# Kernel tuning notes

Hardware: AMD Instinct MI355X
Metric: run time of the kernel (lower is better)

Reference implementation:

```python
import jax, jax.numpy as jnp
import numpy as np

EPS = 1e-5
NV, NF, NV_PREV = 40962, 81920, 10242  # icosphere level 6 / level 5
B, HALF, OUT = 2, 64, 64


def setup_inputs() -> dict:
    key = jax.random.key(0)
    ks = jax.random.split(key, 32)
    rn = lambda i, shape, s=1.0: jax.random.normal(ks[i], shape, dtype=jnp.float32) * s
    ri = lambda i, shape, hi: jax.random.randint(ks[i], shape, 0, hi, dtype=jnp.int32)
    ru = lambda i, shape: jax.random.uniform(ks[i], shape, dtype=jnp.float32, minval=0.5, maxval=1.5)
    s_up = 1.0 / np.sqrt(HALF * 4)   # torch uniform(-stdv, stdv) scale analog
    s_c1 = 1.0 / np.sqrt(2 * HALF)
    s_c3 = 1.0 / np.sqrt(OUT)
    return {
        'x1': rn(0, (B, HALF, NV_PREV)),
        'x2': rn(1, (B, HALF, NV)),
        'G_cols': ri(2, (3 * NF, 3), NV), 'G_vals': rn(3, (3 * NF, 3), 0.1),
        'L_cols': ri(4, (NV, 7), NV), 'L_vals': rn(5, (NV, 7), 0.1),
        'F2V_cols': ri(6, (NV, 6), NF), 'F2V_vals': rn(7, (NV, 6), 0.3),
        'EW': rn(8, (NF, 3)), 'NS': rn(9, (NF, 3)),
        'v2p': jnp.arange(NV_PREV, dtype=jnp.int32),
        'up_coeffs': rn(10, (HALF, HALF, 4), s_up), 'up_bias': rn(11, (HALF,), s_up),
        'c2_coeffs': rn(12, (OUT, OUT, 4), 1.0 / np.sqrt(OUT * 4)), 'c2_bias': rn(13, (OUT,), 1.0 / np.sqrt(OUT * 4)),
        'conv1_w': rn(14, (OUT, 2 * HALF), s_c1), 'conv1_b': rn(15, (OUT,), s_c1),
        'conv3_w': rn(16, (OUT, OUT), s_c3), 'conv3_b': rn(17, (OUT,), s_c3),
        'convs_w': rn(18, (OUT, 2 * HALF), s_c1), 'convs_b': rn(19, (OUT,), s_c1),
        'bn1_g': ru(20, (OUT,)), 'bn1_b': rn(21, (OUT,), 0.1),
        'bn2_g': ru(22, (OUT,)), 'bn2_b': rn(23, (OUT,), 0.1),
        'bn3_g': ru(24, (OUT,)), 'bn3_b': rn(25, (OUT,), 0.1),
        'bns_g': ru(26, (OUT,)), 'bns_b': rn(27, (OUT,), 0.1),
    }


def spmm_ell(x, cols, vals):
    """x: (B,C,V), cols/vals: (R,K) fixed-nnz-per-row sparse matrix -> (B,C,R)."""
    return jnp.einsum('bcrk,rk->bcr', x[:, :, cols], vals)


def mesh_conv(x, coeffs, bias, G_cols, G_vals, L_cols, L_vals, F2V_cols, F2V_vals, EW, NS):
    b, c, v = x.shape
    # gradient on faces: (B,C,3*NF) -> (B,C,NF,3)
    gf = spmm_ell(x, G_cols, G_vals).reshape(b, c, 3, -1).transpose(0, 1, 3, 2)
    lap = spmm_ell(x, L_cols, L_vals)                                 # (B,C,V)
    gv_ew = spmm_ell(jnp.sum(gf * EW, axis=-1), F2V_cols, F2V_vals)   # (B,C,V)
    gv_ns = spmm_ell(jnp.sum(gf * NS, axis=-1), F2V_cols, F2V_vals)   # (B,C,V)
    feat = jnp.stack([x, lap, gv_ew, gv_ns], axis=-1)                 # (B,C,V,4)
    return jnp.einsum('bivk,oik->bov', feat, coeffs) + bias[:, None]


def bn(x, g, b):
    # training-mode BatchNorm1d over (batch, vertex) dims, biased variance
    m = jnp.mean(x, axis=(0, 2), keepdims=True)
    v = jnp.mean((x - m) ** 2, axis=(0, 2), keepdims=True)
    return g[:, None] * (x - m) / jnp.sqrt(v + EPS) + b[:, None]


def pconv(x, w, b):
    # 1x1 Conv1d
    return jnp.einsum('bcv,oc->bov', x, w) + b[:, None]


def reference(x1, x2, G_cols, G_vals, L_cols, L_vals, F2V_cols, F2V_vals, EW, NS, v2p,
              up_coeffs, up_bias, c2_coeffs, c2_bias, conv1_w, conv1_b, conv3_w, conv3_b,
              convs_w, convs_b, bn1_g, bn1_b, bn2_g, bn2_b, bn3_g, bn3_b, bns_g, bns_b):
    sp = (G_cols, G_vals, L_cols, L_vals, F2V_cols, F2V_vals, EW, NS)
    # MeshConv_transpose: pad with ONES (as in torch source) then mesh conv
    b, c, _ = x1.shape
    xin = jnp.ones((b, c, NV), dtype=x1.dtype).at[:, :, v2p].set(x1)
    xu = mesh_conv(xin, up_coeffs, up_bias, *sp)
    x = jnp.concatenate([x2, xu], axis=1)  # (B, in_ch, NV)
    # ResPoolBlock (coarsen=False, diff_chan=True)
    h = jax.nn.relu(bn(pconv(x, conv1_w, conv1_b), bn1_g, bn1_b))
    h = jax.nn.relu(bn(mesh_conv(h, c2_coeffs, c2_bias, *sp), bn2_g, bn2_b))
    h = bn(pconv(h, conv3_w, conv3_b), bn3_g, bn3_b)
    s = bn(pconv(x, convs_w, convs_b), bns_g, bns_b)
    return jax.nn.relu(h + s)
```

## Files before the change

kernel.cpp:

```cpp
#include <hip/hip_runtime.h>

typedef unsigned short u16;
typedef unsigned int u32;

constexpr int kNV  = 40962;
constexpr int kNF  = 81920;
constexpr int kNVP = 10242;
constexpr int kB   = 2;
constexpr float kEPS  = 1e-5f;
constexpr int kBNN   = kB * kNV;
constexpr float kInvN = 1.0f / (float)kBNN;
constexpr int kTiles = (kBNN + 15) / 16;

typedef __attribute__((ext_vector_type(8))) short bf16x8;
typedef __attribute__((ext_vector_type(4))) float f32x4;
union U4 { uint4 u; bf16x8 h; };

__device__ __forceinline__ float bflo(u32 u) { return __uint_as_float(u << 16); }
__device__ __forceinline__ float bfhi(u32 u) { return __uint_as_float(u & 0xffff0000u); }
__device__ __forceinline__ u32 packbf(float a, float b) {
    u32 ua = __float_as_uint(a), ub = __float_as_uint(b);
    ua += 0x7fffu + ((ua >> 16) & 1u);
    ub += 0x7fffu + ((ub >> 16) & 1u);
    return (ua >> 16) | (ub & 0xffff0000u);
}
__device__ __forceinline__ u16 bf16r(float a) {
    u32 ua = __float_as_uint(a);
    ua += 0x7fffu + ((ua >> 16) & 1u);
    return (u16)(ua >> 16);
}
__device__ __forceinline__ float b2f(u16 u) { return __uint_as_float(((u32)u) << 16); }

__global__ void zero_stats_k(float* stats) {
    int t = threadIdx.x;
    if (t < 512) stats[t] = 0.f;
}

__global__ __launch_bounds__(256) void build_facetab_k(
    const int* __restrict__ Gc, const float* __restrict__ Gv,
    const float* __restrict__ ew, const float* __restrict__ ns,
    uint4* __restrict__ tab)
{
    int idx = blockIdx.x * 256 + threadIdx.x;
    if (idx >= kNF * 9) return;
    int f = idx / 9, jk = idx - f * 9;
    int j = jk / 3, k = jk - j * 3;
    int r = j * kNF + f;
    float gv = Gv[r * 3 + k];
    tab[idx] = make_uint4((u32)Gc[r * 3 + k],
                          __float_as_uint(gv * ew[f * 3 + j]),
                          __float_as_uint(gv * ns[f * 3 + j]), 0u);
}

__global__ __launch_bounds__(256) void pack_coeffs_k(const float* __restrict__ coeffs,
                                                     u16* __restrict__ Bg)
{
    int idx = blockIdx.x * 256 + threadIdx.x;
    if (idx >= 256 * 64) return;
    int k = idx >> 6, col = idx & 63;
    int s = k >> 5, kg = (k >> 3) & 3, jj = k & 7;
    Bg[((s * 4 + kg) * 64 + col) * 8 + jj] =
        bf16r(coeffs[((size_t)col * 64 + (k >> 2)) * 4 + (k & 3)]);
}

__global__ __launch_bounds__(256) void transpose_in_k(const float* __restrict__ x1,
                                                      const float* __restrict__ x2,
                                                      u16* __restrict__ xin16,
                                                      u16* __restrict__ Xc) {
    __shared__ float t1[64 * 65];
    __shared__ float t2[64 * 65];
    const int tilesPerB = (kNV + 63) / 64;
    int tile = blockIdx.x % tilesPerB;
    int b    = blockIdx.x / tilesPerB;
    int v0   = tile * 64;
    int tid  = threadIdx.x;
    bool hasX1 = v0 < kNVP;
#pragma unroll
    for (int r = 0; r < 16; ++r) {
        int idx = r * 256 + tid;
        int c = idx >> 6, vl = idx & 63;
        int v = v0 + vl;
        if (v < kNV) {
            t2[vl * 65 + c] = x2[(size_t)(b * 64 + c) * kNV + v];
            if (hasX1) t1[vl * 65 + c] = (v < kNVP) ? x1[(size_t)(b * 64 + c) * kNVP + v] : 1.0f;
        }
    }
    __syncthreads();
#pragma unroll
    for (int r = 0; r < 16; ++r) {
        int idx = r * 256 + tid;
        int vl = idx >> 6, c = idx & 63;
        int v = v0 + vl;
        if (v < kNV) {
            Xc[(size_t)(b * kNV + v) * 128 + c]   = bf16r(t2[vl * 65 + c]);
            xin16[(size_t)(b * kNV + v) * 64 + c] = hasX1 ? bf16r(t1[vl * 65 + c]) : (u16)0x3f80;
        }
    }
}

template <bool BN>
__global__ __launch_bounds__(256) void face_k(
    const u16* __restrict__ src,
    const uint4* __restrict__ tab,
    const float* __restrict__ st, const float* __restrict__ bg, const float* __restrict__ bb,
    u32* __restrict__ gegn)
{
    int lane = threadIdx.x & 63;
    int cl = lane & 31, half = lane >> 5;
    int c0 = 2 * cl;
    int wave = blockIdx.x * 4 + (threadIdx.x >> 6);
    int nW   = gridDim.x * 4;
    float sc0 = 0.f, sh0 = 0.f, sc1 = 0.f, sh1 = 0.f;
    if constexpr (BN) {
        float m0 = st[c0] * kInvN, m1 = st[c0 + 1] * kInvN;
        float v0 = st[64 + c0] * kInvN - m0 * m0;
        float v1 = st[64 + c0 + 1] * kInvN - m1 * m1;
        sc0 = bg[c0] * rsqrtf(v0 + kEPS);     sh0 = bb[c0] - m0 * sc0;
        sc1 = bg[c0 + 1] * rsqrtf(v1 + kEPS); sh1 = bb[c0 + 1] - m1 * sc1;
    }
    const int nG = (kB * kNF) / 8;
    for (int g = wave; g < nG; g += nW) {
        int t0 = g * 8;
#pragma unroll
        for (int p = 0; p < 4; ++p) {
            int task = t0 + 2 * p + half;
            int b = task >= kNF;
            int f = task - (b ? kNF : 0);
            const u16* sb = src + (size_t)b * kNV * 64;
            const uint4* tf = tab + (size_t)f * 9;
            float aE0 = 0.f, aE1 = 0.f, aN0 = 0.f, aN1 = 0.f;
#pragma unroll
            for (int jk = 0; jk < 9; ++jk) {
                uint4 tb = tf[jk];
                float wE = __uint_as_float(tb.y), wN = __uint_as_float(tb.z);
                u32 xv = *(const u32*)&sb[(size_t)tb.x * 64 + c0];
                float x0 = bflo(xv), x1 = bfhi(xv);
                if constexpr (BN) {
                    x0 = fmaf(x0, sc0, sh0); x0 = x0 > 0.f ? x0 : 0.f;
                    x1 = fmaf(x1, sc1, sh1); x1 = x1 > 0.f ? x1 : 0.f;
                }
                aE0 = fmaf(wE, x0, aE0); aE1 = fmaf(wE, x1, aE1);
                aN0 = fmaf(wN, x0, aN0); aN1 = fmaf(wN, x1, aN1);
            }
            *(uint2*)&gegn[(size_t)task * 64 + c0] =
                make_uint2(packbf(aE0, aN0), packbf(aE1, aN1));
        }
    }
}

template <bool STATS, bool BN, bool OUT16>
__global__ __launch_bounds__(256, 2) void vertex_fused_k(
    const u16* __restrict__ src,
    const u32* __restrict__ gegn,
    const int* __restrict__ Lc, const float* __restrict__ Lv,
    const int* __restrict__ Fc, const float* __restrict__ Fv,
    const uint4* __restrict__ Bg,
    const float* __restrict__ bias,
    const float* __restrict__ st, const float* __restrict__ bg, const float* __restrict__ bbn,
    void* __restrict__ out_, int outStride, float* __restrict__ stats)
{
    __shared__ __align__(16) uint2 feat[4][16][64];
    __shared__ float sred[STATS ? 4 * 128 : 4];
    int tid   = threadIdx.x;
    int lane  = tid & 63;
    int cl = lane & 31, half = lane >> 5;
    int c0 = 2 * cl;
    int wslot = tid >> 6;
    float sc0 = 0.f, sh0 = 0.f, sc1 = 0.f, sh1 = 0.f;
    if constexpr (BN) {
        float m0 = st[c0] * kInvN, m1 = st[c0 + 1] * kInvN;
        float v0 = st[64 + c0] * kInvN - m0 * m0;
        float v1 = st[64 + c0 + 1] * kInvN - m1 * m1;
        sc0 = bg[c0] * rsqrtf(v0 + kEPS);     sh0 = bbn[c0] - m0 * sc0;
        sc1 = bg[c0 + 1] * rsqrtf(v1 + kEPS); sh1 = bbn[c0 + 1] - m1 * sc1;
    }
    int tA = lane & 15, kg = lane >> 4;
    const int amask = (tA & 3) << 3;
    float bias_w[4];
#pragma unroll
    for (int nf = 0; nf < 4; ++nf) bias_w[nf] = bias[nf * 16 + tA];
    float s_[4] = {0.f, 0.f, 0.f, 0.f}, sq_[4] = {0.f, 0.f, 0.f, 0.f};

    int wave = blockIdx.x * 4 + wslot;
    int nW   = gridDim.x * 4;

    for (int tile = wave; tile < kTiles; tile += nW) {
        int base = tile * 16;
#pragma unroll 4
        for (int p = 0; p < 8; ++p) {
            int t = 2 * p + half;
            int task = base + t;
            float x0 = 0.f, x1 = 0.f, l0 = 0.f, l1 = 0.f;
            float e0 = 0.f, e1 = 0.f, n0 = 0.f, n1 = 0.f;
            if (task < kBNN) {
                int b = task >= kNV;
                int v = task - (b ? kNV : 0);
                const u16* sb = src + (size_t)b * kNV * 64;
                const u32* gb = gegn + (size_t)b * kNF * 64;
                u32 xv = *(const u32*)&src[(size_t)task * 64 + c0];
                x0 = bflo(xv); x1 = bfhi(xv);
                if constexpr (BN) {
                    x0 = fmaf(x0, sc0, sh0); x0 = x0 > 0.f ? x0 : 0.f;
                    x1 = fmaf(x1, sc1, sh1); x1 = x1 > 0.f ? x1 : 0.f;
                }
#pragma unroll
                for (int k = 0; k < 7; ++k) {
                    int col = Lc[v * 7 + k];
                    float w = Lv[v * 7 + k];
                    u32 lv = *(const u32*)&sb[(size_t)col * 64 + c0];
                    float y0 = bflo(lv), y1 = bfhi(lv);
                    if constexpr (BN) {
                        y0 = fmaf(y0, sc0, sh0); y0 = y0 > 0.f ? y0 : 0.f;
                        y1 = fmaf(y1, sc1, sh1); y1 = y1 > 0.f ? y1 : 0.f;
                    }
                    l0 = fmaf(w, y0, l0); l1 = fmaf(w, y1, l1);
                }
#pragma unroll
                for (int k = 0; k < 6; ++k) {
                    int col = Fc[v * 6 + k];
                    float w = Fv[v * 6 + k];
                    uint2 gv = *(const uint2*)&gb[(size_t)col * 64 + c0];
                    e0 = fmaf(w, bflo(gv.x), e0); n0 = fmaf(w, bfhi(gv.x), n0);
                    e1 = fmaf(w, bflo(gv.y), e1); n1 = fmaf(w, bfhi(gv.y), n1);
                }
            }
            int cs = c0 ^ ((t & 3) << 3);
            *(uint4*)&feat[wslot][t][cs] =
                make_uint4(packbf(x0, l0), packbf(e0, n0), packbf(x1, l1), packbf(e1, n1));
        }
        f32x4 z = {0.f, 0.f, 0.f, 0.f};
        f32x4 acc[4]; acc[0] = z; acc[1] = z; acc[2] = z; acc[3] = z;
#pragma unroll
        for (int sl = 0; sl < 8; ++sl) {
            int i0 = sl * 8 + kg * 2;
            U4 a; a.u = *(const uint4*)&feat[wslot][tA][i0 ^ amask];
#pragma unroll
            for (int nf = 0; nf < 4; ++nf) {
                U4 bb; bb.u = Bg[(sl * 4 + kg) * 64 + nf * 16 + tA];
                acc[nf] = __builtin_amdgcn_mfma_f32_16x16x32_bf16(a.h, bb.h, acc[nf], 0, 0, 0);
            }
        }
#pragma unroll
        for (int nf = 0; nf < 4; ++nf) {
#pragma unroll
            for (int r = 0; r < 4; ++r) {
                int task = base + kg * 4 + r;
                if (task < kBNN) {
                    float val = acc[nf][r] + bias_w[nf];
                    int col = nf * 16 + tA;
                    if constexpr (OUT16)
                        ((u16*)out_)[(size_t)task * outStride + col] = bf16r(val);
                    else
                        ((float*)out_)[(size_t)task * outStride + col] = val;
                    if constexpr (STATS) { s_[nf] += val; sq_[nf] += val * val; }
                }
            }
        }
    }
    if constexpr (STATS) {
#pragma unroll
        for (int nf = 0; nf < 4; ++nf) {
            s_[nf]  += __shfl_xor(s_[nf], 16, 64);  s_[nf]  += __shfl_xor(s_[nf], 32, 64);
            sq_[nf] += __shfl_xor(sq_[nf], 16, 64); sq_[nf] += __shfl_xor(sq_[nf], 32, 64);
        }
        if (lane < 16) {
#pragma unroll
            for (int nf = 0; nf < 4; ++nf) {
                sred[wslot * 128 + nf * 16 + lane]      = s_[nf];
                sred[wslot * 128 + 64 + nf * 16 + lane] = sq_[nf];
            }
        }
        __syncthreads();
        if (wslot == 0) {
            float S = 0.f, SQ = 0.f;
#pragma unroll
            for (int w = 0; w < 4; ++w) {
                S  += sred[w * 128 + lane];
                SQ += sred[w * 128 + 64 + lane];
            }
            atomicAdd(&stats[lane], S);
            atomicAdd(&stats[64 + lane], SQ);
        }
    }
}

__global__ __launch_bounds__(512) void pconv_dual_k(
    const u16* __restrict__ Xc,
    const float* __restrict__ W1, const float* __restrict__ b1,
    const float* __restrict__ W2, const float* __restrict__ b2,
    u16* __restrict__ O1, u16* __restrict__ O2,
    float* __restrict__ stats1, float* __restrict__ stats2)
{
    __shared__ __align__(16) u16 Bl[128 * 128];
    __shared__ float sred[8 * 256];
    int tid = threadIdx.x;
    for (int idx = tid; idx < 128 * 128; idx += 512) {
        int k = idx >> 7, col = idx & 127;
        int s = k >> 5, kg = (k >> 3) & 3, jj = k & 7;
        float v = (col < 64) ? W1[(size_t)col * 128 + k] : W2[(size_t)(col - 64) * 128 + k];
        Bl[((s * 4 + kg) * 128 + (col ^ kg)) * 8 + jj] = bf16r(v);
    }
    __syncthreads();

    int lane = tid & 63, wslot = tid >> 6;
    int tA = lane & 15, kg = lane >> 4;
    float bias_w[8];
#pragma unroll
    for (int nf = 0; nf < 8; ++nf)
        bias_w[nf] = (nf < 4) ? b1[nf * 16 + tA] : b2[(nf - 4) * 16 + tA];
    float s_[8] = {0.f}, sq_[8] = {0.f};

    int wave = blockIdx.x * 8 + wslot;
    int nW   = gridDim.x * 8;
    for (int tile = wave; tile < kTiles; tile += nW) {
        int base = tile * 16;
        int taskA = min(base + tA, kBNN - 1);
        f32x4 zz = {0.f, 0.f, 0.f, 0.f};
        f32x4 acc[8];
#pragma unroll
        for (int nf = 0; nf < 8; ++nf) acc[nf] = zz;
#pragma unroll
        for (int s = 0; s < 4; ++s) {
            U4 a; a.u = *(const uint4*)&Xc[(size_t)taskA * 128 + s * 32 + kg * 8];
#pragma unroll
            for (int nf = 0; nf < 8; ++nf) {
                int colb = nf * 16 + tA;
                U4 bb; bb.u = *(const uint4*)&Bl[((s * 4 + kg) * 128 + (colb ^ kg)) * 8];
                acc[nf] = __builtin_amdgcn_mfma_f32_16x16x32_bf16(a.h, bb.h, acc[nf], 0, 0, 0);
            }
        }
#pragma unroll
        for (int nf = 0; nf < 8; ++nf) {
#pragma unroll
            for (int r = 0; r < 4; ++r) {
                int task = base + kg * 4 + r;
                if (task < kBNN) {
                    float val = acc[nf][r] + bias_w[nf];
                    if (nf < 4) O1[(size_t)task * 64 + nf * 16 + tA] = bf16r(val);
                    else        O2[(size_t)task * 64 + (nf - 4) * 16 + tA] = bf16r(val);
                    s_[nf] += val; sq_[nf] += val * val;
                }
            }
        }
    }
#pragma unroll
    for (int nf = 0; nf < 8; ++nf) {
        s_[nf]  += __shfl_xor(s_[nf], 16, 64);  s_[nf]  += __shfl_xor(s_[nf], 32, 64);
        sq_[nf] += __shfl_xor(sq_[nf], 16, 64); sq_[nf] += __shfl_xor(sq_[nf], 32, 64);
    }
    if (lane < 16) {
#pragma unroll
        for (int nf = 0; nf < 8; ++nf) {
            sred[wslot * 256 + nf * 16 + lane]       = s_[nf];
            sred[wslot * 256 + 128 + nf * 16 + lane] = sq_[nf];
        }
    }
    __syncthreads();
    if (wslot == 0) {
        float S = 0.f, SQ = 0.f;
#pragma unroll
        for (int w = 0; w < 8; ++w) {
            S  += sred[w * 256 + lane];
            SQ += sred[w * 256 + 128 + lane];
        }
        atomicAdd(&stats1[lane], S);
        atomicAdd(&stats1[64 + lane], SQ);
    } else if (wslot == 1) {
        float S = 0.f, SQ = 0.f;
#pragma unroll
        for (int w = 0; w < 8; ++w) {
            S  += sred[w * 256 + 64 + lane];
            SQ += sred[w * 256 + 128 + 64 + lane];
        }
        atomicAdd(&stats2[lane], S);
        atomicAdd(&stats2[64 + lane], SQ);
    }
}

__global__ __launch_bounds__(512) void pconv3_k(
    const u16* __restrict__ P2,
    const float* __restrict__ st2, const float* __restrict__ g2, const float* __restrict__ b2n,
    const float* __restrict__ W, const float* __restrict__ bW,
    u16* __restrict__ O, float* __restrict__ stats)
{
    __shared__ __align__(16) u16 Bl[64 * 64];
    __shared__ float sred[8 * 128];
    int tid = threadIdx.x;
    for (int idx = tid; idx < 64 * 64; idx += 512) {
        int k = idx >> 6, col = idx & 63;
        int s = k >> 5, kg = (k >> 3) & 3, jj = k & 7;
        Bl[((s * 4 + kg) * 64 + (col ^ kg)) * 8 + jj] = bf16r(W[(size_t)col * 64 + k]);
    }
    __syncthreads();

    int lane = tid & 63, wslot = tid >> 6;
    int tA = lane & 15, kg = lane >> 4;
    float scA[2][8], shA[2][8];
#pragma unroll
    for (int s = 0; s < 2; ++s)
#pragma unroll
        for (int j = 0; j < 8; ++j) {
            int ch = s * 32 + kg * 8 + j;
            float m   = st2[ch] * kInvN;
            float var = st2[64 + ch] * kInvN - m * m;
            float sc  = g2[ch] * rsqrtf(var + kEPS);
            scA[s][j] = sc;
            shA[s][j] = b2n[ch] - m * sc;
        }
    float bias_w[4];
#pragma unroll
    for (int nf = 0; nf < 4; ++nf) bias_w[nf] = bW[nf * 16 + tA];
    float s_[4] = {0.f}, sq_[4] = {0.f};

    int wave = blockIdx.x * 8 + wslot;
    int nW   = gridDim.x * 8;
    for (int tile = wave; tile < kTiles; tile += nW) {
        int base = tile * 16;
        int taskA = min(base + tA, kBNN - 1);
        f32x4 zz = {0.f, 0.f, 0.f, 0.f};
        f32x4 acc[4]; acc[0] = zz; acc[1] = zz; acc[2] = zz; acc[3] = zz;
#pragma unroll
        for (int s = 0; s < 2; ++s) {
            U4 raw; raw.u = *(const uint4*)&P2[(size_t)taskA * 64 + s * 32 + kg * 8];
            u32 w_[4];
#pragma unroll
            for (int p = 0; p < 4; ++p) {
                u32 word = (p < 2) ? ((p == 0) ? raw.u.x : raw.u.y) : ((p == 2) ? raw.u.z : raw.u.w);
                float t0 = fmaf(bflo(word), scA[s][2 * p],     shA[s][2 * p]);     t0 = t0 > 0.f ? t0 : 0.f;
                float t1 = fmaf(bfhi(word), scA[s][2 * p + 1], shA[s][2 * p + 1]); t1 = t1 > 0.f ? t1 : 0.f;
                w_[p] = packbf(t0, t1);
            }
            U4 a; a.u = make_uint4(w_[0], w_[1], w_[2], w_[3]);
#pragma unroll
            for (int nf = 0; nf < 4; ++nf) {
                int colb = nf * 16 + tA;
                U4 bb; bb.u = *(const uint4*)&Bl[((s * 4 + kg) * 64 + (colb ^ kg)) * 8];
                acc[nf] = __builtin_amdgcn_mfma_f32_16x16x32_bf16(a.h, bb.h, acc[nf], 0, 0, 0);
            }
        }
#pragma unroll
        for (int nf = 0; nf < 4; ++nf) {
#pragma unroll
            for (int r = 0; r < 4; ++r) {
                int task = base + kg * 4 + r;
                if (task < kBNN) {
                    float val = acc[nf][r] + bias_w[nf];
                    O[(size_t)task * 64 + nf * 16 + tA] = bf16r(val);
                    s_[nf] += val; sq_[nf] += val * val;
                }
            }
        }
    }
#pragma unroll
    for (int nf = 0; nf < 4; ++nf) {
        s_[nf]  += __shfl_xor(s_[nf], 16, 64);  s_[nf]  += __shfl_xor(s_[nf], 32, 64);
        sq_[nf] += __shfl_xor(sq_[nf], 16, 64); sq_[nf] += __shfl_xor(sq_[nf], 32, 64);
    }
    if (lane < 16) {
#pragma unroll
        for (int nf = 0; nf < 4; ++nf) {
            sred[wslot * 128 + nf * 16 + lane]      = s_[nf];
            sred[wslot * 128 + 64 + nf * 16 + lane] = sq_[nf];
        }
    }
    __syncthreads();
    if (wslot == 0) {
        float S = 0.f, SQ = 0.f;
#pragma unroll
        for (int w = 0; w < 8; ++w) {
            S  += sred[w * 128 + lane];
            SQ += sred[w * 128 + 64 + lane];
        }
        atomicAdd(&stats[lane], S);
        atomicAdd(&stats[64 + lane], SQ);
    }
}

__global__ __launch_bounds__(256) void final_k(
    const u16* __restrict__ P3, const u16* __restrict__ S,
    const float* __restrict__ st3, const float* __restrict__ stS,
    const float* __restrict__ g3, const float* __restrict__ b3,
    const float* __restrict__ gs, const float* __restrict__ bs,
    float* __restrict__ out)
{
    __shared__ float lds[64 * 65];
    const int tilesPerB = (kNV + 63) / 64;
    int tile = blockIdx.x % tilesPerB;
    int b    = blockIdx.x / tilesPerB;
    int v0   = tile * 64;
    int tid  = threadIdx.x;
#pragma unroll
    for (int r = 0; r < 16; ++r) {
        int idx = r * 256 + tid;
        int vl = idx >> 6, o = idx & 63;
        int v = v0 + vl;
        if (v < kNV) {
            float m3  = st3[o] * kInvN;
            float vr3 = st3[64 + o] * kInvN - m3 * m3;
            float sc3 = g3[o] * rsqrtf(vr3 + kEPS);
            float sh3 = b3[o] - m3 * sc3;
            float mS  = stS[o] * kInvN;
            float vrS = stS[64 + o] * kInvN - mS * mS;
            float scS = gs[o] * rsqrtf(vrS + kEPS);
            float shS = bs[o] - mS * scS;
            size_t base = (size_t)(b * kNV + v) * 64 + o;
            float val = fmaf(b2f(P3[base]), sc3, sh3) + fmaf(b2f(S[base]), scS, shS);
            lds[vl * 65 + o] = val > 0.f ? val : 0.f;
        }
    }
    __syncthreads();
#pragma unroll
    for (int r = 0; r < 16; ++r) {
        int idx = r * 256 + tid;
        int o = idx >> 6, vl = idx & 63;
        int v = v0 + vl;
        if (v < kNV) out[(size_t)(b * 64 + o) * kNV + v] = lds[vl * 65 + o];
    }
}

extern "C" void kernel_launch(void* const* d_in, const int* in_sizes, int n_in,
                              void* d_out, int out_size, void* d_ws, size_t ws_size,
                              hipStream_t stream) {
    const float* x1  = (const float*)d_in[0];
    const float* x2  = (const float*)d_in[1];
    const int*   Gc  = (const int*)d_in[2];
    const float* Gv  = (const float*)d_in[3];
    const int*   Lc  = (const int*)d_in[4];
    const float* Lv  = (const float*)d_in[5];
    const int*   Fc  = (const int*)d_in[6];
    const float* Fv  = (const float*)d_in[7];
    const float* ew  = (const float*)d_in[8];
    const float* ns  = (const float*)d_in[9];
    const float* upC = (const float*)d_in[11];
    const float* upB = (const float*)d_in[12];
    const float* c2C = (const float*)d_in[13];
    const float* c2B = (const float*)d_in[14];
    const float* w1  = (const float*)d_in[15];
    const float* b1  = (const float*)d_in[16];
    const float* w3  = (const float*)d_in[17];
    const float* b3  = (const float*)d_in[18];
    const float* wsw = (const float*)d_in[19];
    const float* wsb = (const float*)d_in[20];
    const float* bn1g = (const float*)d_in[21];
    const float* bn1b = (const float*)d_in[22];
    const float* bn2g = (const float*)d_in[23];
    const float* bn2b = (const float*)d_in[24];
    const float* bn3g = (const float*)d_in[25];
    const float* bn3b = (const float*)d_in[26];
    const float* bnsg = (const float*)d_in[27];
    const float* bnsb = (const float*)d_in[28];

    float* ws = (float*)d_ws;
    float* stats = ws;
    size_t off = 512;
    u16* Xc    = (u16*)(ws + off); off += (size_t)kBNN * 64;
    u16* xin16 = (u16*)(ws + off); off += (size_t)kBNN * 32;
    u32* gegn  = (u32*)(ws + off); off += (size_t)kB * kNF * 64;
    u16* P1    = (u16*)(ws + off); off += (size_t)kBNN * 32;
    u16* Sbuf  = (u16*)(ws + off); off += (size_t)kBNN * 32;
    u16* P2    = (u16*)(ws + off); off += (size_t)kBNN * 32;
    u16* P3    = (u16*)(ws + off); off += (size_t)kBNN * 32;
    uint4* faceTab = (uint4*)(ws + off); off += (size_t)kNF * 9 * 4;
    u16* BgUp = (u16*)(ws + off); off += 256 * 64 / 2;
    u16* BgC2 = (u16*)(ws + off); off += 256 * 64 / 2;
    float* out = (float*)d_out;

    zero_stats_k<<<1, 512, 0, stream>>>(stats);
    build_facetab_k<<<(kNF * 9 + 255) / 256, 256, 0, stream>>>(Gc, Gv, ew, ns, faceTab);
    pack_coeffs_k<<<64, 256, 0, stream>>>(upC, BgUp);
    pack_coeffs_k<<<64, 256, 0, stream>>>(c2C, BgC2);
    transpose_in_k<<<2 * 641, 256, 0, stream>>>(x1, x2, xin16, Xc);
    face_k<false><<<2048, 256, 0, stream>>>(xin16, faceTab,
                                            nullptr, nullptr, nullptr, gegn);
    vertex_fused_k<false, false, true><<<1280, 256, 0, stream>>>(
        xin16, gegn, Lc, Lv, Fc, Fv, (const uint4*)BgUp, upB,
        nullptr, nullptr, nullptr, (void*)(Xc + 64), 128, nullptr);
    pconv_dual_k<<<512, 512, 0, stream>>>(Xc, w1, b1, wsw, wsb, P1, Sbuf,
                                          stats + 0 * 128, stats + 3 * 128);
    face_k<true><<<2048, 256, 0, stream>>>(P1, faceTab,
                                           stats + 0 * 128, bn1g, bn1b, gegn);
    vertex_fused_k<true, true, true><<<1280, 256, 0, stream>>>(
        P1, gegn, Lc, Lv, Fc, Fv, (const uint4*)BgC2, c2B,
        stats + 0 * 128, bn1g, bn1b, P2, 64, stats + 1 * 128);
    pconv3_k<<<512, 512, 0, stream>>>(P2, stats + 1 * 128, bn2g, bn2b,
                                      w3, b3, P3, stats + 2 * 128);
    final_k<<<2 * 641, 256, 0, stream>>>(P3, Sbuf, stats + 2 * 128, stats + 3 * 128,
                                         bn3g, bn3b, bnsg, bnsb, out);
}
```

Measured before the change: 261.2 us.

## Widen per-lane gathers to four channels and pack vertex sparse tables

```diff
diff --git a/kernel.cpp b/kernel.cpp
--- a/kernel.cpp
+++ b/kernel.cpp
@@ -50,6 +50,28 @@
     tab[idx] = make_uint4((u32)Gc[r * 3 + k],
                           __float_as_uint(gv * ew[f * 3 + j]),
                           __float_as_uint(gv * ns[f * 3 + j]), 0u);
+}
+
+__global__ __launch_bounds__(256) void build_vtab_k(
+    const int* __restrict__ Lc, const float* __restrict__ Lv,
+    const int* __restrict__ Fc, const float* __restrict__ Fv,
+    u32* __restrict__ vtab)
+{
+    int v = blockIdx.x * 256 + threadIdx.x;
+    if (v >= kNV) return;
+    u32* d = vtab + (size_t)v * 32;
+#pragma unroll
+    for (int k = 0; k < 7; ++k) {
+        d[k]      = (u32)Lc[v * 7 + k];
+        d[16 + k] = __float_as_uint(Lv[v * 7 + k]);
+    }
+#pragma unroll
+    for (int k = 0; k < 6; ++k) {
+        d[7 + k]  = (u32)Fc[v * 6 + k];
+        d[23 + k] = __float_as_uint(Fv[v * 6 + k]);
+    }
+    d[13] = 0; d[14] = 0; d[15] = 0;
+    d[29] = 0; d[30] = 0; d[31] = 0;
 }
 
 __global__ __launch_bounds__(256) void pack_coeffs_k(const float* __restrict__ coeffs,
@@ -106,44 +128,48 @@
     u32* __restrict__ gegn)
 {
     int lane = threadIdx.x & 63;
-    int cl = lane & 31, half = lane >> 5;
-    int c0 = 2 * cl;
+    int q  = lane >> 4;
+    int c0 = 4 * (lane & 15);
     int wave = blockIdx.x * 4 + (threadIdx.x >> 6);
     int nW   = gridDim.x * 4;
-    float sc0 = 0.f, sh0 = 0.f, sc1 = 0.f, sh1 = 0.f;
+    float sc[4], sh[4];
     if constexpr (BN) {
-        float m0 = st[c0] * kInvN, m1 = st[c0 + 1] * kInvN;
-        float v0 = st[64 + c0] * kInvN - m0 * m0;
-        float v1 = st[64 + c0 + 1] * kInvN - m1 * m1;
-        sc0 = bg[c0] * rsqrtf(v0 + kEPS);     sh0 = bb[c0] - m0 * sc0;
-        sc1 = bg[c0 + 1] * rsqrtf(v1 + kEPS); sh1 = bb[c0 + 1] - m1 * sc1;
-    }
-    const int nG = (kB * kNF) / 8;
+#pragma unroll
+        for (int j = 0; j < 4; ++j) {
+            float m   = st[c0 + j] * kInvN;
+            float var = st[64 + c0 + j] * kInvN - m * m;
+            sc[j] = bg[c0 + j] * rsqrtf(var + kEPS);
+            sh[j] = bb[c0 + j] - m * sc[j];
+        }
+    }
+    const int nG = (kB * kNF) / 16;
     for (int g = wave; g < nG; g += nW) {
-        int t0 = g * 8;
+        int t0 = g * 16;
 #pragma unroll
         for (int p = 0; p < 4; ++p) {
-            int task = t0 + 2 * p + half;
+            int task = t0 + 4 * p + q;
             int b = task >= kNF;
             int f = task - (b ? kNF : 0);
             const u16* sb = src + (size_t)b * kNV * 64;
             const uint4* tf = tab + (size_t)f * 9;
-            float aE0 = 0.f, aE1 = 0.f, aN0 = 0.f, aN1 = 0.f;
+            float aE[4] = {0.f, 0.f, 0.f, 0.f}, aN[4] = {0.f, 0.f, 0.f, 0.f};
 #pragma unroll
             for (int jk = 0; jk < 9; ++jk) {
                 uint4 tb = tf[jk];
                 float wE = __uint_as_float(tb.y), wN = __uint_as_float(tb.z);
-                u32 xv = *(const u32*)&sb[(size_t)tb.x * 64 + c0];
-                float x0 = bflo(xv), x1 = bfhi(xv);
-                if constexpr (BN) {
-                    x0 = fmaf(x0, sc0, sh0); x0 = x0 > 0.f ? x0 : 0.f;
-                    x1 = fmaf(x1, sc1, sh1); x1 = x1 > 0.f ? x1 : 0.f;
+                uint2 xv = *(const uint2*)&sb[(size_t)tb.x * 64 + c0];
+                float x_[4] = {bflo(xv.x), bfhi(xv.x), bflo(xv.y), bfhi(xv.y)};
+#pragma unroll
+                for (int j = 0; j < 4; ++j) {
+                    float x = x_[j];
+                    if constexpr (BN) { x = fmaf(x, sc[j], sh[j]); x = x > 0.f ? x : 0.f; }
+                    aE[j] = fmaf(wE, x, aE[j]);
+                    aN[j] = fmaf(wN, x, aN[j]);
                 }
-                aE0 = fmaf(wE, x0, aE0); aE1 = fmaf(wE, x1, aE1);
-                aN0 = fmaf(wN, x0, aN0); aN1 = fmaf(wN, x1, aN1);
-            }
-            *(uint2*)&gegn[(size_t)task * 64 + c0] =
-                make_uint2(packbf(aE0, aN0), packbf(aE1, aN1));
+            }
+            *(uint4*)&gegn[(size_t)task * 64 + c0] =
+                make_uint4(packbf(aE[0], aN[0]), packbf(aE[1], aN[1]),
+                           packbf(aE[2], aN[2]), packbf(aE[3], aN[3]));
         }
     }
 }
@@ -152,8 +178,7 @@
 __global__ __launch_bounds__(256, 2) void vertex_fused_k(
     const u16* __restrict__ src,
     const u32* __restrict__ gegn,
-    const int* __restrict__ Lc, const float* __restrict__ Lv,
-    const int* __restrict__ Fc, const float* __restrict__ Fv,
+    const u32* __restrict__ vtab,
     const uint4* __restrict__ Bg,
     const float* __restrict__ bias,
     const float* __restrict__ st, const float* __restrict__ bg, const float* __restrict__ bbn,
@@ -163,16 +188,18 @@
     __shared__ float sred[STATS ? 4 * 128 : 4];
     int tid   = threadIdx.x;
     int lane  = tid & 63;
-    int cl = lane & 31, half = lane >> 5;
-    int c0 = 2 * cl;
+    int q  = lane >> 4;
+    int c0 = 4 * (lane & 15);
     int wslot = tid >> 6;
-    float sc0 = 0.f, sh0 = 0.f, sc1 = 0.f, sh1 = 0.f;
+    float sc[4], sh[4];
     if constexpr (BN) {
-        float m0 = st[c0] * kInvN, m1 = st[c0 + 1] * kInvN;
-        float v0 = st[64 + c0] * kInvN - m0 * m0;
-        float v1 = st[64 + c0 + 1] * kInvN - m1 * m1;
-        sc0 = bg[c0] * rsqrtf(v0 + kEPS);     sh0 = bbn[c0] - m0 * sc0;
-        sc1 = bg[c0 + 1] * rsqrtf(v1 + kEPS); sh1 = bbn[c0 + 1] - m1 * sc1;
+#pragma unroll
+        for (int j = 0; j < 4; ++j) {
+            float m   = st[c0 + j] * kInvN;
+            float var = st[64 + c0 + j] * kInvN - m * m;
+            sc[j] = bg[c0 + j] * rsqrtf(var + kEPS);
+            sh[j] = bbn[c0 + j] - m * sc[j];
+        }
     }
     int tA = lane & 15, kg = lane >> 4;
     const int amask = (tA & 3) << 3;
@@ -186,47 +213,68 @@
 
     for (int tile = wave; tile < kTiles; tile += nW) {
         int base = tile * 16;
-#pragma unroll 4
-        for (int p = 0; p < 8; ++p) {
-            int t = 2 * p + half;
+#pragma unroll
+        for (int p = 0; p < 4; ++p) {
+            int t = 4 * p + q;
             int task = base + t;
-            float x0 = 0.f, x1 = 0.f, l0 = 0.f, l1 = 0.f;
-            float e0 = 0.f, e1 = 0.f, n0 = 0.f, n1 = 0.f;
+            float x_[4] = {0.f, 0.f, 0.f, 0.f}, l_[4] = {0.f, 0.f, 0.f, 0.f};
+            float e_[4] = {0.f, 0.f, 0.f, 0.f}, n_[4] = {0.f, 0.f, 0.f, 0.f};
             if (task < kBNN) {
                 int b = task >= kNV;
                 int v = task - (b ? kNV : 0);
                 const u16* sb = src + (size_t)b * kNV * 64;
                 const u32* gb = gegn + (size_t)b * kNF * 64;
-                u32 xv = *(const u32*)&src[(size_t)task * 64 + c0];
-                x0 = bflo(xv); x1 = bfhi(xv);
-                if constexpr (BN) {
-                    x0 = fmaf(x0, sc0, sh0); x0 = x0 > 0.f ? x0 : 0.f;
-                    x1 = fmaf(x1, sc1, sh1); x1 = x1 > 0.f ? x1 : 0.f;
+                const u32* vt = vtab + (size_t)v * 32;
+                uint4  I0 = *(const uint4*)&vt[0];
+                uint4  I1 = *(const uint4*)&vt[4];
+                uint4  I2 = *(const uint4*)&vt[8];
+                u32    I3 = vt[12];
+                float4 W0 = *(const float4*)&vt[16];
+                float4 W1 = *(const float4*)&vt[20];
+                float4 W2 = *(const float4*)&vt[24];
+                float  W3 = __uint_as_float(vt[28]);
+                u32 Lcols[7] = {I0.x, I0.y, I0.z, I0.w, I1.x, I1.y, I1.z};
+                float Lw[7]  = {W0.x, W0.y, W0.z, W0.w, W1.x, W1.y, W1.z};
+                u32 Fcols[6] = {I1.w, I2.x, I2.y, I2.z, I2.w, I3};
+                float Fw[6]  = {W1.w, W2.x, W2.y, W2.z, W2.w, W3};
+
+                uint2 xv = *(const uint2*)&src[(size_t)task * 64 + c0];
+                float xr[4] = {bflo(xv.x), bfhi(xv.x), bflo(xv.y), bfhi(xv.y)};
+#pragma unroll
+                for (int j = 0; j < 4; ++j) {
+                    float x = xr[j];
+                    if constexpr (BN) { x = fmaf(x, sc[j], sh[j]); x = x > 0.f ? x : 0.f; }
+                    x_[j] = x;
                 }
 #pragma unroll
                 for (int k = 0; k < 7; ++k) {
-                    int col = Lc[v * 7 + k];
-                    float w = Lv[v * 7 + k];
-                    u32 lv = *(const u32*)&sb[(size_t)col * 64 + c0];
-                    float y0 = bflo(lv), y1 = bfhi(lv);
-                    if constexpr (BN) {
-                        y0 = fmaf(y0, sc0, sh0); y0 = y0 > 0.f ? y0 : 0.f;
-                        y1 = fmaf(y1, sc1, sh1); y1 = y1 > 0.f ? y1 : 0.f;
+                    uint2 lv = *(const uint2*)&sb[(size_t)Lcols[k] * 64 + c0];
+                    float w = Lw[k];
+                    float yr[4] = {bflo(lv.x), bfhi(lv.x), bflo(lv.y), bfhi(lv.y)};
+#pragma unroll
+                    for (int j = 0; j < 4; ++j) {
+                        float y = yr[j];
+                        if constexpr (BN) { y = fmaf(y, sc[j], sh[j]); y = y > 0.f ? y : 0.f; }
+                        l_[j] = fmaf(w, y, l_[j]);
                     }
-                    l0 = fmaf(w, y0, l0); l1 = fmaf(w, y1, l1);
                 }
 #pragma unroll
                 for (int k = 0; k < 6; ++k) {
-                    int col = Fc[v * 6 + k];
-                    float w = Fv[v * 6 + k];
-                    uint2 gv = *(const uint2*)&gb[(size_t)col * 64 + c0];
-                    e0 = fmaf(w, bflo(gv.x), e0); n0 = fmaf(w, bfhi(gv.x), n0);
-                    e1 = fmaf(w, bflo(gv.y), e1); n1 = fmaf(w, bfhi(gv.y), n1);
+                    uint4 gv = *(const uint4*)&gb[(size_t)Fcols[k] * 64 + c0];
+                    float w = Fw[k];
+                    e_[0] = fmaf(w, bflo(gv.x), e_[0]); n_[0] = fmaf(w, bfhi(gv.x), n_[0]);
+                    e_[1] = fmaf(w, bflo(gv.y), e_[1]); n_[1] = fmaf(w, bfhi(gv.y), n_[1]);
+                    e_[2] = fmaf(w, bflo(gv.z), e_[2]); n_[2] = fmaf(w, bfhi(gv.z), n_[2]);
+                    e_[3] = fmaf(w, bflo(gv.w), e_[3]); n_[3] = fmaf(w, bfhi(gv.w), n_[3]);
                 }
             }
             int cs = c0 ^ ((t & 3) << 3);
             *(uint4*)&feat[wslot][t][cs] =
-                make_uint4(packbf(x0, l0), packbf(e0, n0), packbf(x1, l1), packbf(e1, n1));
+                make_uint4(packbf(x_[0], l_[0]), packbf(e_[0], n_[0]),
+                           packbf(x_[1], l_[1]), packbf(e_[1], n_[1]));
+            *(uint4*)&feat[wslot][t][cs + 2] =
+                make_uint4(packbf(x_[2], l_[2]), packbf(e_[2], n_[2]),
+                           packbf(x_[3], l_[3]), packbf(e_[3], n_[3]));
         }
         f32x4 z = {0.f, 0.f, 0.f, 0.f};
         f32x4 acc[4]; acc[0] = z; acc[1] = z; acc[2] = z; acc[3] = z;
@@ -561,26 +609,28 @@
     u16* P2    = (u16*)(ws + off); off += (size_t)kBNN * 32;
     u16* P3    = (u16*)(ws + off); off += (size_t)kBNN * 32;
     uint4* faceTab = (uint4*)(ws + off); off += (size_t)kNF * 9 * 4;
+    u32* vtab  = (u32*)(ws + off); off += (size_t)kNV * 32;
     u16* BgUp = (u16*)(ws + off); off += 256 * 64 / 2;
     u16* BgC2 = (u16*)(ws + off); off += 256 * 64 / 2;
     float* out = (float*)d_out;
 
     zero_stats_k<<<1, 512, 0, stream>>>(stats);
     build_facetab_k<<<(kNF * 9 + 255) / 256, 256, 0, stream>>>(Gc, Gv, ew, ns, faceTab);
+    build_vtab_k<<<(kNV + 255) / 256, 256, 0, stream>>>(Lc, Lv, Fc, Fv, vtab);
     pack_coeffs_k<<<64, 256, 0, stream>>>(upC, BgUp);
     pack_coeffs_k<<<64, 256, 0, stream>>>(c2C, BgC2);
     transpose_in_k<<<2 * 641, 256, 0, stream>>>(x1, x2, xin16, Xc);
-    face_k<false><<<2048, 256, 0, stream>>>(xin16, faceTab,
+    face_k<false><<<2560, 256, 0, stream>>>(xin16, faceTab,
                                             nullptr, nullptr, nullptr, gegn);
     vertex_fused_k<false, false, true><<<1280, 256, 0, stream>>>(
-        xin16, gegn, Lc, Lv, Fc, Fv, (const uint4*)BgUp, upB,
+        xin16, gegn, vtab, (const uint4*)BgUp, upB,
         nullptr, nullptr, nullptr, (void*)(Xc + 64), 128, nullptr);
     pconv_dual_k<<<512, 512, 0, stream>>>(Xc, w1, b1, wsw, wsb, P1, Sbuf,
                                           stats + 0 * 128, stats + 3 * 128);
-    face_k<true><<<2048, 256, 0, stream>>>(P1, faceTab,
+    face_k<true><<<2560, 256, 0, stream>>>(P1, faceTab,
                                            stats + 0 * 128, bn1g, bn1b, gegn);
     vertex_fused_k<true, true, true><<<1280, 256, 0, stream>>>(
-        P1, gegn, Lc, Lv, Fc, Fv, (const uint4*)BgC2, c2B,
+        P1, gegn, vtab, (const uint4*)BgC2, c2B,
         stats + 0 * 128, bn1g, bn1b, P2, 64, stats + 1 * 128);
     pconv3_k<<<512, 512, 0, stream>>>(P2, stats + 1 * 128, bn2g, bn2b,
                                       w3, b3, P3, stats + 2 * 128);
```

After: 262.8 us. Within noise of the previous version (+0.6%).
